# Kernel tuning notes

Hardware: AMD Instinct MI355X
Metric: run time of the kernel (lower is better)

## Reference

```python
import jax, jax.numpy as jnp
import numpy as np

B, L, F, H, K = 2048, 256, 64, 32, 2  # batch, seq len, features, g_hidden, LocalHilDim

def _dense_init(key, fan_in, fan_out):
    return (jax.random.normal(key, (fan_in, fan_out), jnp.float32) / np.sqrt(fan_in).astype(np.float32))

def setup_inputs() -> dict:
    key = jax.random.key(0)
    ks = jax.random.split(key, 12)
    s = jax.random.randint(ks[0], (B, L), 0, K)
    g = jax.random.normal(ks[1], (B,), jnp.float32)
    return dict(
        s=s, g=g,
        W_emb=_dense_init(ks[2], K, F), b_emb=jnp.zeros((F,), jnp.float32),
        W_g1=_dense_init(ks[3], 1, H), b_g1=jnp.zeros((H,), jnp.float32),
        W_g2=_dense_init(ks[4], H, F), b_g2=jnp.zeros((F,), jnp.float32),
        W_gh=_dense_init(ks[5], 1, F), b_gh=jnp.zeros((F,), jnp.float32),
        W_gc=_dense_init(ks[6], 1, F), b_gc=jnp.zeros((F,), jnp.float32),
        Wi=_dense_init(ks[7], F, 4 * F),  # fused input->gates (flax LSTMCell ii/if/ig/io, no bias)
        Wh=_dense_init(ks[8], F, 4 * F),  # fused hidden->gates (hi/hf/hg/ho)
        b_lstm=jnp.zeros((4 * F,), jnp.float32),  # fused gate biases
        W_amp=_dense_init(ks[9], F, K), b_amp=jnp.zeros((K,), jnp.float32),
    )

def reference(s, g, W_emb, b_emb, W_g1, b_g1, W_g2, b_g2, W_gh, b_gh, W_gc, b_gc, Wi, Wh, b_lstm, W_amp, b_amp):
    logProbFactor = 1.0
    g_in = g[:, None]                                            # [B,1]
    g_vec = jnp.tanh(g_in @ W_g1 + b_g1) @ W_g2 + b_g2          # g_mlp -> [B,F]
    h0 = g_in @ W_gh + b_gh                                      # init_carry h [B,F]
    c0 = g_in @ W_gc + b_gc                                      # init_carry c [B,F]
    s_pad = jnp.pad(s, ((0, 0), (1, 0)))                         # [B,L+1], leading 0 token
    seqy = jax.nn.one_hot(s_pad, K, dtype=jnp.float32)           # [B,L+1,K]
    emb = seqy @ W_emb + b_emb + g_vec[:, None, :]               # [B,L+1,F]
    # precompute input-side gate projections once: [B,L+1,4F]
    x_proj = emb @ Wi + b_lstm

    def step(carry, xt):                                         # xt: [B,4F]
        h, c = carry
        z = xt + h @ Wh
        zi, zf, zg, zo = jnp.split(z, 4, axis=-1)
        c = jax.nn.sigmoid(zf) * c + jax.nn.sigmoid(zi) * jnp.tanh(zg)
        h = jax.nn.sigmoid(zo) * jnp.tanh(c)
        return (h, c), h

    _, ys = jax.lax.scan(step, (h0, c0), jnp.swapaxes(x_proj, 0, 1))  # ys: [L+1,B,F]
    y = jnp.swapaxes(ys, 0, 1)                                   # [B,L+1,F]
    logits = y[:, :-1, :] @ W_amp + b_amp                        # [B,L,K]
    logp = jax.nn.log_softmax(logits) * logProbFactor
    token_logp = jnp.take_along_axis(logp, s[..., None], axis=-1)[..., 0]  # [B,L]
    return token_logp.sum(axis=-1)                               # [B]
```

## Files before the change

### kernel.cpp

```cpp
#include <hip/hip_runtime.h>


typedef __attribute__((ext_vector_type(8))) short bf16x8;
typedef __attribute__((ext_vector_type(4))) float f32x4;

#define L2E 1.44269504088896340736f
#define LN2 0.69314718055994530942f

__device__ __forceinline__ short f2bf(float x) {
    unsigned u = __builtin_bit_cast(unsigned, x);
    unsigned r = (u + 0x7FFFu + ((u >> 16) & 1u)) >> 16;
    return (short)r;
}

__global__ __launch_bounds__(256) void lstm_kernel(
    const int* __restrict__ s, const float* __restrict__ g,
    const float* __restrict__ W_emb, const float* __restrict__ b_emb,
    const float* __restrict__ W_g1, const float* __restrict__ b_g1,
    const float* __restrict__ W_g2, const float* __restrict__ b_g2,
    const float* __restrict__ W_gh, const float* __restrict__ b_gh,
    const float* __restrict__ W_gc, const float* __restrict__ b_gc,
    const float* __restrict__ Wi, const float* __restrict__ Wh,
    const float* __restrict__ b_lstm, const float* __restrict__ W_amp,
    const float* __restrict__ b_amp, float* __restrict__ out)
{
    __shared__ float Bx[35 * 256];
    __shared__ unsigned char sp_l[260];
    __shared__ __align__(16) short Hb[2][640];
    __shared__ __align__(16) float dLb[256 * 8];
    __shared__ float red2[8][32];

    const int tid = threadIdx.x;
    const int w   = tid >> 6;
    const int l   = tid & 63;
    const int n2  = l & 15;
    const int q   = l >> 4;
    const int wgb = blockIdx.x * 8;

    {
        const int n = tid;
        const float sc = (n >= 128 && n < 192) ? (-2.0f * L2E) : (-L2E);
        float acc[35];
        #pragma unroll
        for (int i = 0; i < 35; ++i) acc[i] = 0.f;
        for (int f = 0; f < 64; ++f) {
            float wi = Wi[f * 256 + n] * sc;
            #pragma unroll
            for (int k = 0; k < 32; ++k) acc[k] += W_g2[k * 64 + f] * wi;
            acc[32] += W_emb[f] * wi;
            acc[33] += W_emb[64 + f] * wi;
            acc[34] += (b_emb[f] + b_g2[f]) * wi;
        }
        acc[34] += b_lstm[n] * sc;
        #pragma unroll
        for (int i = 0; i < 35; ++i) Bx[i * 256 + n] = acc[i];
        unsigned v = 0;
        #pragma unroll
        for (int b = 0; b < 8; ++b)
            v |= (unsigned)(s[(wgb + b) * 256 + n] & 1) << b;
        sp_l[n + 1] = (unsigned char)v;
        if (n == 0) sp_l[0] = 0;
    }
    __syncthreads();

    bf16x8 Bf[4][2];
    float  Dsel[4];
    f32x4  C0b[4];
    {
        bf16x8 B2f[4];
        float c0add[4];
        #pragma unroll
        for (int gi = 0; gi < 4; ++gi) {
            const int n = gi * 64 + w * 16 + n2;
            const float scg = (gi == 2) ? (-2.0f * L2E) : (-L2E);
            #pragma unroll
            for (int kf = 0; kf < 2; ++kf)
                #pragma unroll
                for (int j = 0; j < 8; ++j)
                    Bf[gi][kf][j] = f2bf(Wh[(kf * 32 + q * 8 + j) * 256 + n] * scg);
            #pragma unroll
            for (int j = 0; j < 8; ++j)
                B2f[gi][j] = f2bf(Bx[(q * 8 + j) * 256 + n]);
            c0add[gi] = Bx[32 * 256 + n] + Bx[34 * 256 + n];
            Dsel[gi]  = Bx[33 * 256 + n] - Bx[32 * 256 + n];
        }
        const float g_a = g[wgb + ((l & 15) >> 1)];
        bf16x8 Atv;
        #pragma unroll
        for (int j = 0; j < 8; ++j) {
            int k = q * 8 + j;
            Atv[j] = f2bf(tanhf(g_a * W_g1[k] + b_g1[k]));
        }
        const f32x4 zero4 = {0.f, 0.f, 0.f, 0.f};
        #pragma unroll
        for (int gi = 0; gi < 4; ++gi) {
            f32x4 c = __builtin_amdgcn_mfma_f32_16x16x32_bf16(Atv, B2f[gi], zero4, 0, 0, 0);
            float cvA = c[0] + c0add[gi];
            float cvB = c[2] + c0add[gi];
            C0b[gi][0] = cvA; C0b[gi][1] = cvA; C0b[gi][2] = cvB; C0b[gi][3] = cvB;
        }
    }
    bf16x8 BLd0, BLd1;
    f32x4 CL0;
    {
        #pragma unroll
        for (int j = 0; j < 8; ++j) {
            int k = q * 8 + j;
            BLd0[j] = (n2 == 0) ? f2bf(W_amp[k * 2 + 1] - W_amp[k * 2]) : (short)0;
            BLd1[j] = (n2 == 0) ? f2bf(W_amp[(k + 32) * 2 + 1] - W_amp[(k + 32) * 2]) : (short)0;
        }
        float bd = (n2 == 0) ? (b_amp[1] - b_amp[0]) : 0.f;
        CL0[0] = bd; CL0[1] = bd; CL0[2] = bd; CL0[3] = bd;
    }

    const int fcol   = w * 16 + n2;
    const int bA     = q * 2;
    const int bB     = bA + 1;
    const int haddrA = bA * 80 + fcol;
    const int haddrB = haddrA + 80;
    float csA, csB;
    {
        float gA = g[wgb + bA], gB = g[wgb + bB];
        csA = (-2.0f * L2E) * (gA * W_gc[fcol] + b_gc[fcol]);
        csB = (-2.0f * L2E) * (gB * W_gc[fcol] + b_gc[fcol]);
        Hb[0][haddrA] = f2bf(gA * W_gh[fcol] + b_gh[fcol]);
        Hb[0][haddrB] = f2bf(gB * W_gh[fcol] + b_gh[fcol]);
    }
    __syncthreads();

    const int ra = ((l & 15) >> 1) * 80 + q * 8;
    unsigned spt = 0;

    auto step = [&](int t, int rb, int slot, bool doGate) {
        bf16x8 a0 = *(const bf16x8*)&Hb[rb][ra];
        bf16x8 a1 = *(const bf16x8*)&Hb[rb][ra + 32];
        unsigned spt_n = sp_l[t + 1];
        const float fA = (float)((spt >> bA) & 1u);
        const float fB = (float)((spt >> bB) & 1u);

        f32x4 acc[4];
        #pragma unroll
        for (int gi = 0; gi < 4; ++gi) {
            f32x4 a = __builtin_amdgcn_mfma_f32_16x16x32_bf16(a1, Bf[gi][1], C0b[gi], 0, 0, 0);
            acc[gi] = __builtin_amdgcn_mfma_f32_16x16x32_bf16(a0, Bf[gi][0], a, 0, 0, 0);
        }

        const bool rr = (w == slot) && (t >= 1);
        if (rr) {
            f32x4 aL = __builtin_amdgcn_mfma_f32_16x16x32_bf16(a1, BLd1, CL0, 0, 0, 0);
            aL = __builtin_amdgcn_mfma_f32_16x16x32_bf16(a0, BLd0, aL, 0, 0, 0);
            if (n2 == 0) {
                float2 d2; d2.x = aL[0]; d2.y = aL[2];
                *(float2*)&dLb[(t - 1) * 8 + 2 * q] = d2;
            }
        }

        if (doGate) {
            float yiA = __builtin_fmaf(fA, Dsel[0], acc[0][0]);
            float yiB = __builtin_fmaf(fB, Dsel[0], acc[0][2]);
            float yfA = __builtin_fmaf(fA, Dsel[1], acc[1][0]);
            float yfB = __builtin_fmaf(fB, Dsel[1], acc[1][2]);
            float ygA = __builtin_fmaf(fA, Dsel[2], acc[2][0]);
            float ygB = __builtin_fmaf(fB, Dsel[2], acc[2][2]);
            float yoA = __builtin_fmaf(fA, Dsel[3], acc[3][0]);
            float yoB = __builtin_fmaf(fB, Dsel[3], acc[3][2]);
            float siA = __builtin_amdgcn_rcpf(1.0f + __builtin_amdgcn_exp2f(yiA));
            float siB = __builtin_amdgcn_rcpf(1.0f + __builtin_amdgcn_exp2f(yiB));
            float sfA = __builtin_amdgcn_rcpf(1.0f + __builtin_amdgcn_exp2f(yfA));
            float sfB = __builtin_amdgcn_rcpf(1.0f + __builtin_amdgcn_exp2f(yfB));
            float rgA = __builtin_amdgcn_rcpf(1.0f + __builtin_amdgcn_exp2f(ygA));
            float rgB = __builtin_amdgcn_rcpf(1.0f + __builtin_amdgcn_exp2f(ygB));
            float soA = __builtin_amdgcn_rcpf(1.0f + __builtin_amdgcn_exp2f(yoA));
            float soB = __builtin_amdgcn_rcpf(1.0f + __builtin_amdgcn_exp2f(yoB));
            float tgsA = __builtin_fmaf(-4.0f * L2E, rgA, 2.0f * L2E);
            float tgsB = __builtin_fmaf(-4.0f * L2E, rgB, 2.0f * L2E);
            csA = __builtin_fmaf(sfA, csA, siA * tgsA);
            csB = __builtin_fmaf(sfB, csB, siB * tgsB);
            float so2A = soA + soA;
            float so2B = soB + soB;
            float r5A = __builtin_amdgcn_rcpf(1.0f + __builtin_amdgcn_exp2f(csA));
            float r5B = __builtin_amdgcn_rcpf(1.0f + __builtin_amdgcn_exp2f(csB));
            float hA  = __builtin_fmaf(so2A, r5A, -soA);
            float hB  = __builtin_fmaf(so2B, r5B, -soB);
            unsigned hv;
            asm("v_cvt_pk_bf16_f32 %0, %1, %2" : "=v"(hv) : "v"(hA), "v"(hB));
            Hb[1 - rb][haddrA] = (short)hv;
            Hb[1 - rb][haddrB] = (short)(hv >> 16);
        }
        spt = spt_n;
        __syncthreads();
    };

    for (int t0 = 0; t0 < 256; t0 += 4) {
        step(t0 + 0, 0, 0, true);
        step(t0 + 1, 1, 1, true);
        step(t0 + 2, 0, 2, true);
        step(t0 + 3, 1, 3, true);
    }
    step(256, 0, 0, false);

    {
        unsigned bits = (unsigned)sp_l[tid + 1];
        f32x4 v0 = *(const f32x4*)&dLb[tid * 8];
        f32x4 v1 = *(const f32x4*)&dLb[tid * 8 + 4];
        f32x4 s0, s1;
        #pragma unroll
        for (int r = 0; r < 4; ++r) {
            float x0 = ((bits >> r) & 1u) ? -v0[r] : v0[r];
            s0[r] = __builtin_amdgcn_logf(1.0f + __builtin_amdgcn_exp2f(L2E * x0));
            float x1 = ((bits >> (r + 4)) & 1u) ? -v1[r] : v1[r];
            s1[r] = __builtin_amdgcn_logf(1.0f + __builtin_amdgcn_exp2f(L2E * x1));
        }
        *(f32x4*)&dLb[tid * 8]     = s0;
        *(f32x4*)&dLb[tid * 8 + 4] = s1;
        __syncthreads();
        {
            int b = tid >> 5, j = tid & 31;
            float sum = 0.f;
            #pragma unroll
            for (int k = 0; k < 8; ++k)
                sum += dLb[(j * 8 + k) * 8 + b];
            red2[b][j] = sum;
        }
        __syncthreads();
        if (tid < 8) {
            float sum = 0.f;
            #pragma unroll
            for (int j2 = 0; j2 < 32; ++j2) sum += red2[tid][j2];
            out[wgb + tid] = -LN2 * sum;
        }
    }
}

extern "C" void kernel_launch(void* const* d_in, const int* in_sizes, int n_in,
                              void* d_out, int out_size, void* d_ws, size_t ws_size,
                              hipStream_t stream) {
    (void)in_sizes; (void)n_in; (void)out_size; (void)d_ws; (void)ws_size;
    const int*   s      = (const int*)d_in[0];
    const float* g      = (const float*)d_in[1];
    const float* W_emb  = (const float*)d_in[2];
    const float* b_emb  = (const float*)d_in[3];
    const float* W_g1   = (const float*)d_in[4];
    const float* b_g1   = (const float*)d_in[5];
    const float* W_g2   = (const float*)d_in[6];
    const float* b_g2   = (const float*)d_in[7];
    const float* W_gh   = (const float*)d_in[8];
    const float* b_gh   = (const float*)d_in[9];
    const float* W_gc   = (const float*)d_in[10];
    const float* b_gc   = (const float*)d_in[11];
    const float* Wi     = (const float*)d_in[12];
    const float* Wh     = (const float*)d_in[13];
    const float* b_lstm = (const float*)d_in[14];
    const float* W_amp  = (const float*)d_in[15];
    const float* b_amp  = (const float*)d_in[16];
    float* out = (float*)d_out;

    lstm_kernel<<<256, 256, 0, stream>>>(s, g, W_emb, b_emb, W_g1, b_g1, W_g2, b_g2,
                                         W_gh, b_gh, W_gc, b_gc, Wi, Wh, b_lstm,
                                         W_amp, b_amp, out);
}
```

Measured before the change: 194.3 us.

## Split LSTM across 512 two-wave blocks of four batch rows each

Halves the batch rows per block from eight to four and the threads per block from 256 to 128, launching 512 blocks so more CUs hold a sequence. Each wave now computes 32 feature columns through eight MFMA tiles per step instead of four, and the MFMA row mapping is remapped to four batch rows. The aim is to use more of the GPU's compute units and to shorten the per-step barrier across fewer waves. In exchange, each wave issues twice as many MFMAs per serial step, and the per-block weight precompute is duplicated across twice as many blocks.

```diff
diff --git a/kernel.cpp b/kernel.cpp
--- a/kernel.cpp
+++ b/kernel.cpp
@@ -13,7 +13,7 @@
     return (short)r;
 }
 
-__global__ __launch_bounds__(256) void lstm_kernel(
+__global__ __launch_bounds__(128) void lstm_kernel(
     const int* __restrict__ s, const float* __restrict__ g,
     const float* __restrict__ W_emb, const float* __restrict__ b_emb,
     const float* __restrict__ W_g1, const float* __restrict__ b_g1,
@@ -26,19 +26,18 @@
 {
     __shared__ float Bx[35 * 256];
     __shared__ unsigned char sp_l[260];
-    __shared__ __align__(16) short Hb[2][640];
-    __shared__ __align__(16) float dLb[256 * 8];
-    __shared__ float red2[8][32];
+    __shared__ __align__(16) short Hb[2][320];
+    __shared__ __align__(16) float dLb[256 * 4];
+    __shared__ float red2[4][32];
 
     const int tid = threadIdx.x;
     const int w   = tid >> 6;
     const int l   = tid & 63;
     const int n2  = l & 15;
     const int q   = l >> 4;
-    const int wgb = blockIdx.x * 8;
-
-    {
-        const int n = tid;
+    const int wgb = blockIdx.x * 4;
+
+    for (int n = tid; n < 256; n += 128) {
         const float sc = (n >= 128 && n < 192) ? (-2.0f * L2E) : (-L2E);
         float acc[35];
         #pragma unroll
@@ -56,35 +55,36 @@
         for (int i = 0; i < 35; ++i) Bx[i * 256 + n] = acc[i];
         unsigned v = 0;
         #pragma unroll
-        for (int b = 0; b < 8; ++b)
+        for (int b = 0; b < 4; ++b)
             v |= (unsigned)(s[(wgb + b) * 256 + n] & 1) << b;
         sp_l[n + 1] = (unsigned char)v;
-        if (n == 0) sp_l[0] = 0;
-    }
+    }
+    if (tid == 0) sp_l[0] = 0;
     __syncthreads();
 
-    bf16x8 Bf[4][2];
-    float  Dsel[4];
-    f32x4  C0b[4];
-    {
-        bf16x8 B2f[4];
-        float c0add[4];
-        #pragma unroll
-        for (int gi = 0; gi < 4; ++gi) {
-            const int n = gi * 64 + w * 16 + n2;
-            const float scg = (gi == 2) ? (-2.0f * L2E) : (-L2E);
+    bf16x8 Bf[8][2];
+    float  Dsel[8];
+    f32x4  C0b[8];
+    {
+        bf16x8 B2f[8];
+        float c0add[8];
+        #pragma unroll
+        for (int m = 0; m < 8; ++m) {
+            const int gt = m >> 1, h = m & 1;
+            const int n  = gt * 64 + w * 32 + h * 16 + n2;
+            const float scg = (gt == 2) ? (-2.0f * L2E) : (-L2E);
             #pragma unroll
             for (int kf = 0; kf < 2; ++kf)
                 #pragma unroll
                 for (int j = 0; j < 8; ++j)
-                    Bf[gi][kf][j] = f2bf(Wh[(kf * 32 + q * 8 + j) * 256 + n] * scg);
+                    Bf[m][kf][j] = f2bf(Wh[(kf * 32 + q * 8 + j) * 256 + n] * scg);
             #pragma unroll
             for (int j = 0; j < 8; ++j)
-                B2f[gi][j] = f2bf(Bx[(q * 8 + j) * 256 + n]);
-            c0add[gi] = Bx[32 * 256 + n] + Bx[34 * 256 + n];
-            Dsel[gi]  = Bx[33 * 256 + n] - Bx[32 * 256 + n];
-        }
-        const float g_a = g[wgb + ((l & 15) >> 1)];
+                B2f[m][j] = f2bf(Bx[(q * 8 + j) * 256 + n]);
+            c0add[m] = Bx[32 * 256 + n] + Bx[34 * 256 + n];
+            Dsel[m]  = Bx[33 * 256 + n] - Bx[32 * 256 + n];
+        }
+        const float g_a = g[wgb + ((l & 15) >> 2)];
         bf16x8 Atv;
         #pragma unroll
         for (int j = 0; j < 8; ++j) {
@@ -93,11 +93,10 @@
         }
         const f32x4 zero4 = {0.f, 0.f, 0.f, 0.f};
         #pragma unroll
-        for (int gi = 0; gi < 4; ++gi) {
-            f32x4 c = __builtin_amdgcn_mfma_f32_16x16x32_bf16(Atv, B2f[gi], zero4, 0, 0, 0);
-            float cvA = c[0] + c0add[gi];
-            float cvB = c[2] + c0add[gi];
-            C0b[gi][0] = cvA; C0b[gi][1] = cvA; C0b[gi][2] = cvB; C0b[gi][3] = cvB;
+        for (int m = 0; m < 8; ++m) {
+            f32x4 c = __builtin_amdgcn_mfma_f32_16x16x32_bf16(Atv, B2f[m], zero4, 0, 0, 0);
+            float cv = c[0] + c0add[m];
+            C0b[m][0] = cv; C0b[m][1] = cv; C0b[m][2] = cv; C0b[m][3] = cv;
         }
     }
     bf16x8 BLd0, BLd1;
@@ -113,57 +112,52 @@
         CL0[0] = bd; CL0[1] = bd; CL0[2] = bd; CL0[3] = bd;
     }
 
-    const int fcol   = w * 16 + n2;
-    const int bA     = q * 2;
-    const int bB     = bA + 1;
-    const int haddrA = bA * 80 + fcol;
-    const int haddrB = haddrA + 80;
+    const int fA = w * 32 + n2, fB = fA + 16;
+    const int haddrA = q * 80 + fA;
+    const int haddrB = q * 80 + fB;
     float csA, csB;
     {
-        float gA = g[wgb + bA], gB = g[wgb + bB];
-        csA = (-2.0f * L2E) * (gA * W_gc[fcol] + b_gc[fcol]);
-        csB = (-2.0f * L2E) * (gB * W_gc[fcol] + b_gc[fcol]);
-        Hb[0][haddrA] = f2bf(gA * W_gh[fcol] + b_gh[fcol]);
-        Hb[0][haddrB] = f2bf(gB * W_gh[fcol] + b_gh[fcol]);
+        float gq = g[wgb + q];
+        csA = (-2.0f * L2E) * (gq * W_gc[fA] + b_gc[fA]);
+        csB = (-2.0f * L2E) * (gq * W_gc[fB] + b_gc[fB]);
+        Hb[0][haddrA] = f2bf(gq * W_gh[fA] + b_gh[fA]);
+        Hb[0][haddrB] = f2bf(gq * W_gh[fB] + b_gh[fB]);
     }
     __syncthreads();
 
-    const int ra = ((l & 15) >> 1) * 80 + q * 8;
+    const int ra = ((l & 15) >> 2) * 80 + q * 8;
     unsigned spt = 0;
 
     auto step = [&](int t, int rb, int slot, bool doGate) {
         bf16x8 a0 = *(const bf16x8*)&Hb[rb][ra];
         bf16x8 a1 = *(const bf16x8*)&Hb[rb][ra + 32];
         unsigned spt_n = sp_l[t + 1];
-        const float fA = (float)((spt >> bA) & 1u);
-        const float fB = (float)((spt >> bB) & 1u);
-
-        f32x4 acc[4];
-        #pragma unroll
-        for (int gi = 0; gi < 4; ++gi) {
-            f32x4 a = __builtin_amdgcn_mfma_f32_16x16x32_bf16(a1, Bf[gi][1], C0b[gi], 0, 0, 0);
-            acc[gi] = __builtin_amdgcn_mfma_f32_16x16x32_bf16(a0, Bf[gi][0], a, 0, 0, 0);
+        const float fq = (float)((spt >> q) & 1u);
+
+        f32x4 acc[8];
+        #pragma unroll
+        for (int m = 0; m < 8; ++m) {
+            f32x4 a = __builtin_amdgcn_mfma_f32_16x16x32_bf16(a1, Bf[m][1], C0b[m], 0, 0, 0);
+            acc[m] = __builtin_amdgcn_mfma_f32_16x16x32_bf16(a0, Bf[m][0], a, 0, 0, 0);
         }
 
         const bool rr = (w == slot) && (t >= 1);
         if (rr) {
             f32x4 aL = __builtin_amdgcn_mfma_f32_16x16x32_bf16(a1, BLd1, CL0, 0, 0, 0);
             aL = __builtin_amdgcn_mfma_f32_16x16x32_bf16(a0, BLd0, aL, 0, 0, 0);
-            if (n2 == 0) {
-                float2 d2; d2.x = aL[0]; d2.y = aL[2];
-                *(float2*)&dLb[(t - 1) * 8 + 2 * q] = d2;
-            }
+            if (n2 == 0)
+                dLb[(t - 1) * 4 + q] = aL[0];
         }
 
         if (doGate) {
-            float yiA = __builtin_fmaf(fA, Dsel[0], acc[0][0]);
-            float yiB = __builtin_fmaf(fB, Dsel[0], acc[0][2]);
-            float yfA = __builtin_fmaf(fA, Dsel[1], acc[1][0]);
-            float yfB = __builtin_fmaf(fB, Dsel[1], acc[1][2]);
-            float ygA = __builtin_fmaf(fA, Dsel[2], acc[2][0]);
-            float ygB = __builtin_fmaf(fB, Dsel[2], acc[2][2]);
-            float yoA = __builtin_fmaf(fA, Dsel[3], acc[3][0]);
-            float yoB = __builtin_fmaf(fB, Dsel[3], acc[3][2]);
+            float yiA = __builtin_fmaf(fq, Dsel[0], acc[0][0]);
+            float yiB = __builtin_fmaf(fq, Dsel[1], acc[1][0]);
+            float yfA = __builtin_fmaf(fq, Dsel[2], acc[2][0]);
+            float yfB = __builtin_fmaf(fq, Dsel[3], acc[3][0]);
+            float ygA = __builtin_fmaf(fq, Dsel[4], acc[4][0]);
+            float ygB = __builtin_fmaf(fq, Dsel[5], acc[5][0]);
+            float yoA = __builtin_fmaf(fq, Dsel[6], acc[6][0]);
+            float yoB = __builtin_fmaf(fq, Dsel[7], acc[7][0]);
             float siA = __builtin_amdgcn_rcpf(1.0f + __builtin_amdgcn_exp2f(yiA));
             float siB = __builtin_amdgcn_rcpf(1.0f + __builtin_amdgcn_exp2f(yiB));
             float sfA = __builtin_amdgcn_rcpf(1.0f + __builtin_amdgcn_exp2f(yfA));
@@ -191,39 +185,36 @@
         __syncthreads();
     };
 
-    for (int t0 = 0; t0 < 256; t0 += 4) {
-        step(t0 + 0, 0, 0, true);
-        step(t0 + 1, 1, 1, true);
-        step(t0 + 2, 0, 2, true);
-        step(t0 + 3, 1, 3, true);
+    step(0, 0, 0, true);
+    for (int t0 = 1; t0 < 256; t0 += 2) {
+        step(t0, 1, 1, true);
+        step(t0 + 1, 0, 0, true);
     }
     step(256, 0, 0, false);
 
     {
-        unsigned bits = (unsigned)sp_l[tid + 1];
-        f32x4 v0 = *(const f32x4*)&dLb[tid * 8];
-        f32x4 v1 = *(const f32x4*)&dLb[tid * 8 + 4];
-        f32x4 s0, s1;
-        #pragma unroll
-        for (int r = 0; r < 4; ++r) {
-            float x0 = ((bits >> r) & 1u) ? -v0[r] : v0[r];
-            s0[r] = __builtin_amdgcn_logf(1.0f + __builtin_amdgcn_exp2f(L2E * x0));
-            float x1 = ((bits >> (r + 4)) & 1u) ? -v1[r] : v1[r];
-            s1[r] = __builtin_amdgcn_logf(1.0f + __builtin_amdgcn_exp2f(L2E * x1));
-        }
-        *(f32x4*)&dLb[tid * 8]     = s0;
-        *(f32x4*)&dLb[tid * 8 + 4] = s1;
+        for (int u = tid; u < 256; u += 128) {
+            unsigned bits = (unsigned)sp_l[u + 1];
+            f32x4 v = *(const f32x4*)&dLb[u * 4];
+            f32x4 so;
+            #pragma unroll
+            for (int r = 0; r < 4; ++r) {
+                float x = ((bits >> r) & 1u) ? -v[r] : v[r];
+                so[r] = __builtin_amdgcn_logf(1.0f + __builtin_amdgcn_exp2f(L2E * x));
+            }
+            *(f32x4*)&dLb[u * 4] = so;
+        }
         __syncthreads();
         {
             int b = tid >> 5, j = tid & 31;
             float sum = 0.f;
             #pragma unroll
             for (int k = 0; k < 8; ++k)
-                sum += dLb[(j * 8 + k) * 8 + b];
+                sum += dLb[(j * 8 + k) * 4 + b];
             red2[b][j] = sum;
         }
         __syncthreads();
-        if (tid < 8) {
+        if (tid < 4) {
             float sum = 0.f;
             #pragma unroll
             for (int j2 = 0; j2 < 32; ++j2) sum += red2[tid][j2];
@@ -255,7 +246,7 @@
     const float* b_amp  = (const float*)d_in[16];
     float* out = (float*)d_out;
 
-    lstm_kernel<<<256, 256, 0, stream>>>(s, g, W_emb, b_emb, W_g1, b_g1, W_g2, b_g2,
+    lstm_kernel<<<512, 128, 0, stream>>>(s, g, W_emb, b_emb, W_g1, b_g1, W_g2, b_g2,
                                          W_gh, b_gh, W_gc, b_gc, Wi, Wh, b_lstm,
                                          W_amp, b_amp, out);
 }
```

Measured after the change: 234.7 us. 1.21x slower.
